# Kernel optimization log

Hardware: AMD Instinct MI355X
Metric: run time of the kernel (lower is better)

## Reference

```python
import jax, jax.numpy as jnp
import numpy as np

B = 64
IN_CH = 256
CH = 128
OUT_CH = 256
RES = 16
EMBED = 64
N_EMBED = 1024
N_PHYLO = 64          # n_phylo_channels; non-phylo = CH - N_PHYLO = 64
CODES = 16            # codes_per_phylolevel
LEVELS = 4            # n_phylolevels == n_levels_non_attribute
BETA = 0.25
FLAT_IN = N_PHYLO * RES * RES          # 16384
FLAT_Z = EMBED * CODES * LEVELS        # 4096


def setup_inputs() -> dict:
    key = jax.random.key(0)
    ks = jax.random.split(key, 16)
    s = 0.02
    return {
        "x": jax.random.normal(ks[0], (B, IN_CH, RES, RES), jnp.float32),
        "conv_in_w": jax.random.normal(ks[1], (IN_CH, CH), jnp.float32) * s,
        "conv_in_b": jnp.zeros((CH,), jnp.float32),
        "ln_p_g": jnp.ones((N_PHYLO, RES, RES), jnp.float32),
        "ln_p_b": jnp.zeros((N_PHYLO, RES, RES), jnp.float32),
        "W_in_p": jax.random.normal(ks[2], (FLAT_IN, FLAT_Z), jnp.float32) * s,
        "b_in_p": jnp.zeros((FLAT_Z,), jnp.float32),
        "ln_n_g": jnp.ones((CH - N_PHYLO, RES, RES), jnp.float32),
        "ln_n_b": jnp.zeros((CH - N_PHYLO, RES, RES), jnp.float32),
        "W_in_n": jax.random.normal(ks[3], (FLAT_IN, FLAT_Z), jnp.float32) * s,
        "b_in_n": jnp.zeros((FLAT_Z,), jnp.float32),
        "codebook": jax.random.uniform(ks[4], (N_EMBED, EMBED), jnp.float32, -1.0 / N_EMBED, 1.0 / N_EMBED),
        "W_out_p": jax.random.normal(ks[5], (FLAT_Z, FLAT_IN), jnp.float32) * s,
        "b_out_p": jnp.zeros((FLAT_IN,), jnp.float32),
        "W_out_n": jax.random.normal(ks[6], (FLAT_Z, FLAT_IN), jnp.float32) * s,
        "b_out_n": jnp.zeros((FLAT_IN,), jnp.float32),
        "conv_out_w": jax.random.normal(ks[7], (CH, OUT_CH), jnp.float32) * s,
        "conv_out_b": jnp.zeros((OUT_CH,), jnp.float32),
    }


def _layernorm(h, g, b, eps=1e-5):
    # normalize over (C,H,W) per sample, affine params shaped (C,H,W)
    m = jnp.mean(h, axis=(1, 2, 3), keepdims=True)
    v = jnp.var(h, axis=(1, 2, 3), keepdims=True)
    return (h - m) * jax.lax.rsqrt(v + eps) * g + b


def _quantize(z, codebook, beta=BETA):
    # z: (B, E, C, L) treated as (b, c, h, w) by taming VQ
    zp = jnp.transpose(z, (0, 2, 3, 1))                       # (B, C, L, E)
    zf = zp.reshape(-1, zp.shape[-1])                          # (B*C*L, E)
    d = (jnp.sum(zf * zf, axis=1, keepdims=True)
         - 2.0 * zf @ codebook.T
         + jnp.sum(codebook * codebook, axis=1)[None, :])      # (N_tok, n_embed)
    idx = jnp.argmin(d, axis=1)
    zq = codebook[idx].reshape(zp.shape)
    sg = jax.lax.stop_gradient
    loss = jnp.mean((sg(zq) - zp) ** 2) + beta * jnp.mean((zq - sg(zp)) ** 2)
    zq = zp + sg(zq - zp)                                      # straight-through
    return jnp.transpose(zq, (0, 3, 1, 2)), loss


def reference(x, conv_in_w, conv_in_b, ln_p_g, ln_p_b, W_in_p, b_in_p,
              ln_n_g, ln_n_b, W_in_n, b_in_n, codebook,
              W_out_p, b_out_p, W_out_n, b_out_n, conv_out_w, conv_out_b):
    # conv_in: 1x1 conv + SiLU
    h = jax.nn.silu(jnp.einsum('bchw,cd->bdhw', x, conv_in_w) + conv_in_b[None, :, None, None])
    h_phylo, h_img = h[:, :N_PHYLO], h[:, N_PHYLO:]

    # mlp_in (LayerNorm -> Flatten -> Linear -> Unflatten)
    z_p = (_layernorm(h_phylo, ln_p_g, ln_p_b).reshape(B, -1) @ W_in_p + b_in_p).reshape(B, EMBED, CODES, LEVELS)
    z_n = (_layernorm(h_img, ln_n_g, ln_n_b).reshape(B, -1) @ W_in_n + b_in_n).reshape(B, EMBED, CODES, LEVELS)

    zq_p, loss_p = _quantize(z_p, codebook)
    zq_n, loss_n = _quantize(z_n, codebook)
    quant_loss = loss_p + loss_n

    # mlp_out (Flatten -> Linear -> Unflatten)
    hout_p = (zq_p.reshape(B, -1) @ W_out_p + b_out_p).reshape(B, N_PHYLO, RES, RES)
    hout_n = (zq_n.reshape(B, -1) @ W_out_n + b_out_n).reshape(B, CH - N_PHYLO, RES, RES)
    h_ = jnp.concatenate([hout_p, hout_n], axis=1)

    # conv_out: SiLU -> 1x1 conv
    out = jnp.einsum('bchw,cd->bdhw', jax.nn.silu(h_), conv_out_w) + conv_out_b[None, :, None, None]
    return out, quant_loss
```

## Files before the change

kernel.cpp:

```cpp
#include <hip/hip_runtime.h>
#include <hip/hip_bf16.h>
#include <math.h>

#define BB 64
#define IN_CH 256
#define CH 128
#define OUT_CH 256
#define SP 256
#define EMBED 64
#define N_EMBED 1024
#define NPH 64
#define FLAT_IN 16384
#define FLAT_Z 4096

typedef short bf16x8 __attribute__((ext_vector_type(8)));
typedef float f32x4 __attribute__((ext_vector_type(4)));

__device__ __forceinline__ float silu_f(float x){ return x / (1.0f + expf(-x)); }

__device__ __forceinline__ void gl_lds16(const void* g, void* l){
  __builtin_amdgcn_global_load_lds(
      (const __attribute__((address_space(1))) void*)g,
      (__attribute__((address_space(3))) void*)l, 16, 0, 0);
}

__global__ __launch_bounds__(256) void k_fused_in(const float* __restrict__ x,
    const float* __restrict__ w1, const float* __restrict__ b1,
    const float* __restrict__ gp, const float* __restrict__ bp,
    const float* __restrict__ gn, const float* __restrict__ bnl,
    __hip_bfloat16* __restrict__ Ahi)
{
  int b = blockIdx.x, ws = blockIdx.y;
  int t = threadIdx.x;
  int d0 = ws*64;
  float acc[64];
  #pragma unroll
  for (int j=0;j<64;j++) acc[j] = b1[d0+j];
  const float* xb = x + (size_t)b*IN_CH*SP + t;
  for (int c=0;c<IN_CH;c++){
    float xv = xb[(size_t)c*SP];
    #pragma unroll
    for (int j=0;j<64;j++) acc[j] = fmaf(xv, w1[c*CH + d0 + j], acc[j]);
  }
  double s1=0.0, s2=0.0;
  #pragma unroll
  for (int j=0;j<64;j++){
    float v = silu_f(acc[j]);
    acc[j] = v;
    double dv = (double)v;
    s1 += dv; s2 += dv*dv;
  }
  __shared__ double l1[256], l2[256];
  l1[t]=s1; l2[t]=s2; __syncthreads();
  for (int s=128; s>0; s>>=1){
    if (t<s){ l1[t]+=l1[t+s]; l2[t]+=l2[t+s]; }
    __syncthreads();
  }
  double m = l1[0]/(double)FLAT_IN;
  double v = l2[0]/(double)FLAT_IN - m*m;
  float mf = (float)m;
  float rs = (float)(1.0/sqrt(v+1e-5));
  const float* g  = ws? gn : gp;
  const float* bb = ws? bnl: bp;
  __hip_bfloat16* oh = Ahi + ((size_t)ws*64 + b)*FLAT_IN;
  #pragma unroll 4
  for (int j=0;j<64;j++){
    int k = j*256 + t;
    float val = fmaf((acc[j]-mf)*rs, g[k], bb[k]);
    oh[k] = __float2bfloat16(val);
  }
}

template<int N, int K>
__global__ __launch_bounds__(256) void k_gemm_mfma(
    const __hip_bfloat16* __restrict__ A,
    const float* __restrict__ W0, const float* __restrict__ W1,
    float* __restrict__ part, int CHUNK, int KC)
{
  __shared__ float wlds[2*4096];
  __shared__ float alds[2*1024];
  int nt = blockIdx.x, kc = blockIdx.y, wsel = blockIdx.z;
  const float* W = wsel ? W1 : W0;
  int t = threadIdx.x;
  int wave = t >> 6, lane = t & 63;
  int rl = lane & 15;
  int g  = lane >> 4;
  int kg = g * 8;
  int nbase = nt*128;
  int k0 = kc*CHUNK;

  const __hip_bfloat16* Aw = A + (size_t)wsel*64*K;

  int s_lane = ((g&1)<<4) | ((g&2)<<1);
  int wbase0 = kg*128 + ((wave*32 + rl) ^ s_lane);
  int wbase1 = kg*128 + ((wave*32 + 16 + rl) ^ s_lane);
  int abyte[4];
  #pragma unroll
  for (int mf=0; mf<4; ++mf)
    abyte[mf] = (mf*16+rl)*64 + ((g ^ ((rl>>1)&3))<<4);

  int src_off[4]; int dst_base[4];
  #pragma unroll
  for (int i=0;i<4;i++){
    int fi = (i*4+wave)*256 + lane*4;
    int kl = fi>>7, nn = fi&127;
    int s = (((kl>>3)&1)<<4) | (((kl>>3)&2)<<1);
    src_off[i] = kl*N + nbase + (nn ^ s);
    dst_base[i] = (i*4+wave)*256;
  }
  size_t a_src = (size_t)(t>>2)*K + (size_t)(((t&3)^((t>>3)&3))*8);
  int a_dst = wave*256;

  f32x4 acc[4][2];
  #pragma unroll
  for (int mf=0; mf<4; ++mf){ acc[mf][0] = (f32x4){0,0,0,0}; acc[mf][1] = (f32x4){0,0,0,0}; }

  auto STAGE = [&](int buf, int ks){
    const float* Wr = W + (size_t)(k0 + ks*32)*N;
    float* lb = &wlds[buf*4096];
    #pragma unroll
    for (int i=0;i<4;i++) gl_lds16(Wr + src_off[i], lb + dst_base[i]);
    gl_lds16(Aw + a_src + (size_t)(k0 + ks*32), &alds[buf*1024] + a_dst);
  };

  int NT_ = CHUNK/32;
  STAGE(0, 0);

  for (int ks=0; ks<NT_; ++ks){
    int cur = ks & 1;
    int ksn = (ks+1 < NT_) ? ks+1 : ks;
    STAGE(cur^1, ksn);
    __builtin_amdgcn_sched_barrier(0);
    asm volatile("s_waitcnt vmcnt(5)" ::: "memory");
    __builtin_amdgcn_s_barrier();
    __builtin_amdgcn_sched_barrier(0);

    const float* lb = &wlds[cur*4096];
    const char* ab = (const char*)&alds[cur*1024];
    bf16x8 ah[4];
    #pragma unroll
    for (int mf=0; mf<4; ++mf) ah[mf] = *(const bf16x8*)(ab + abyte[mf]);
    float wv0[8], wv1[8];
    #pragma unroll
    for (int j=0;j<8;j++){ wv0[j] = lb[wbase0 + j*128]; wv1[j] = lb[wbase1 + j*128]; }
    bf16x8 bh0, bh1;
    #pragma unroll
    for (int j=0;j<8;j++){
      bh0[j] = __builtin_bit_cast(short, __float2bfloat16(wv0[j]));
      bh1[j] = __builtin_bit_cast(short, __float2bfloat16(wv1[j]));
    }
    #pragma unroll
    for (int mf=0; mf<4; ++mf){
      acc[mf][0] = __builtin_amdgcn_mfma_f32_16x16x32_bf16(ah[mf], bh0, acc[mf][0], 0,0,0);
      acc[mf][1] = __builtin_amdgcn_mfma_f32_16x16x32_bf16(ah[mf], bh1, acc[mf][1], 0,0,0);
    }
    __builtin_amdgcn_sched_barrier(0);
    __builtin_amdgcn_s_barrier();
  }
  asm volatile("s_waitcnt vmcnt(0)" ::: "memory");

  float* P = part + ((size_t)((wsel*KC + kc)*64))*N + nbase + wave*32 + rl;
  #pragma unroll
  for (int mf=0; mf<4; ++mf)
    #pragma unroll
    for (int f=0; f<2; ++f)
      #pragma unroll
      for (int r=0; r<4; ++r)
        P[((size_t)(mf*16 + g*4 + r))*N + f*16] = acc[mf][f][r];
}

__global__ __launch_bounds__(256) void k_zreduce(const float* __restrict__ part,
  const float* __restrict__ bp, const float* __restrict__ bn,
  float* __restrict__ z, int KC)
{
  int idx = blockIdx.x*256 + threadIdx.x;
  int ws = idx >> 18; int rem = idx & 262143;
  int m = rem >> 12; int n = rem & 4095;
  float s = (ws? bn: bp)[n];
  const float* p = part + ((size_t)ws*KC*64 + m)*4096 + n;
  for (int kc=0;kc<KC;kc++) s += p[(size_t)kc*64*4096];
  z[idx] = s;
}

__global__ __launch_bounds__(256) void k_cc(const float* __restrict__ cb, float* __restrict__ cc){
  int j = blockIdx.x*256 + threadIdx.x;
  if (j >= N_EMBED) return;
  float s=0.f;
  for (int e=0;e<EMBED;e++){ float c = cb[(size_t)j*EMBED+e]; s = fmaf(c,c,s); }
  cc[j]=s;
}

__global__ __launch_bounds__(256) void k_qscan(const float* __restrict__ z,
  const float* __restrict__ cb, const float* __restrict__ cc,
  float* __restrict__ bests, int* __restrict__ bestj)
{
  int r = blockIdx.x*256 + threadIdx.x;
  int cs = blockIdx.y;
  int ws = r>>12, rem = r&4095; int b = rem>>6, rr = rem&63;
  const float* zr = z + (size_t)ws*BB*FLAT_Z + (size_t)b*FLAT_Z + rr;
  float zr_[EMBED];
  #pragma unroll
  for (int e=0;e<EMBED;e++) zr_[e] = zr[(size_t)e*64];
  float best = 3.4e38f; int bj = 0;
  int j0 = cs*64;
  for (int jj=0;jj<64;jj++){
    int j = j0 + jj;
    const float* c = cb + (size_t)j*EMBED;
    float s1 = 0.f;
    #pragma unroll
    for (int e=0;e<EMBED;e++) s1 = fmaf(c[e], zr_[e], s1);
    float s = fmaf(-2.f, s1, cc[j]);
    if (s < best){ best = s; bj = j; }
  }
  bests[(size_t)cs*8192 + r] = best;
  bestj[(size_t)cs*8192 + r] = bj;
}

__global__ __launch_bounds__(256) void k_qfin(const float* __restrict__ z,
  const float* __restrict__ cb, const float* __restrict__ bests, const int* __restrict__ bestj,
  __hip_bfloat16* __restrict__ zqA, float* __restrict__ row_sse)
{
  int r = blockIdx.x*256 + threadIdx.x;
  float best = 3.4e38f; int bj = 0;
  for (int cs=0;cs<16;cs++){
    float v = bests[(size_t)cs*8192 + r];
    int j = bestj[(size_t)cs*8192 + r];
    if (v < best){ best=v; bj=j; }
  }
  int ws = r>>12, rem = r&4095; int b = rem>>6, rr = rem&63;
  const float* zr = z + (size_t)ws*BB*FLAT_Z + (size_t)b*FLAT_Z + rr;
  const float* c = cb + (size_t)bj*EMBED;
  __hip_bfloat16* zq = zqA + ((size_t)ws*64 + b)*FLAT_Z;
  float sse = 0.f;
  #pragma unroll
  for (int e=0;e<EMBED;e++){
    float cv = c[e];
    float zv = zr[(size_t)e*64];
    float d = cv - zv; sse = fmaf(d,d,sse);
    zq[(size_t)e*64 + rr] = __float2bfloat16(cv);
  }
  row_sse[r] = sse;
}

__global__ __launch_bounds__(256) void k_loss(const float* __restrict__ row_sse, float* __restrict__ out){
  __shared__ double l[256];
  double s=0.0;
  for (int i=threadIdx.x;i<8192;i+=256) s += (double)row_sse[i];
  l[threadIdx.x]=s; __syncthreads();
  for (int st=128;st>0;st>>=1){ if (threadIdx.x<st) l[threadIdx.x]+=l[threadIdx.x+st]; __syncthreads(); }
  if (threadIdx.x==0) out[(size_t)BB*OUT_CH*SP] = (float)(l[0]*1.25/262144.0);
}

__global__ __launch_bounds__(256) void k_hreduce(const float* __restrict__ part,
  const float* __restrict__ bp, const float* __restrict__ bn,
  float* __restrict__ hbuf, int KC)
{
  int idx = blockIdx.x*256 + threadIdx.x;
  int ws = idx >> 20; int rem = idx & 1048575;
  int m = rem >> 14; int n = rem & 16383;
  float s = (ws? bn: bp)[n];
  const float* p = part + ((size_t)ws*KC*64 + m)*16384 + n;
  for (int kc=0;kc<KC;kc++) s += p[(size_t)kc*64*16384];
  hbuf[((size_t)m*CH + ws*NPH + (n>>8))*SP + (n&255)] = s;
}

__global__ __launch_bounds__(256) void k_conv_out(const float* __restrict__ hbuf,
  const float* __restrict__ w2, const float* __restrict__ b2, float* __restrict__ out)
{
  int b = blockIdx.x, dg = blockIdx.y;
  int p = threadIdx.x;
  int d0 = dg*64;
  float acc[64];
  #pragma unroll
  for (int j=0;j<64;j++) acc[j]=b2[d0+j];
  const float* hb = hbuf + (size_t)b*CH*SP + p;
  for (int c=0;c<CH;c++){
    float hv = silu_f(hb[(size_t)c*SP]);
    #pragma unroll
    for (int j=0;j<64;j++) acc[j] = fmaf(hv, w2[c*OUT_CH + d0 + j], acc[j]);
  }
  float* ob = out + (size_t)b*OUT_CH*SP + (size_t)d0*SP + p;
  #pragma unroll
  for (int j=0;j<64;j++) ob[(size_t)j*SP] = acc[j];
}

extern "C" void kernel_launch(void* const* d_in, const int* in_sizes, int n_in,
                              void* d_out, int out_size, void* d_ws, size_t ws_size,
                              hipStream_t stream)
{
  const float* x   = (const float*)d_in[0];
  const float* w1  = (const float*)d_in[1];
  const float* b1  = (const float*)d_in[2];
  const float* gp  = (const float*)d_in[3];
  const float* bp  = (const float*)d_in[4];
  const float* Wip = (const float*)d_in[5];
  const float* bip = (const float*)d_in[6];
  const float* gn  = (const float*)d_in[7];
  const float* bnl = (const float*)d_in[8];
  const float* Win = (const float*)d_in[9];
  const float* bin = (const float*)d_in[10];
  const float* cb  = (const float*)d_in[11];
  const float* Wop = (const float*)d_in[12];
  const float* bop = (const float*)d_in[13];
  const float* Won = (const float*)d_in[14];
  const float* bon = (const float*)d_in[15];
  const float* w2  = (const float*)d_in[16];
  const float* b2  = (const float*)d_in[17];
  float* out = (float*)d_out;
  float* ws  = (float*)d_ws;

  __hip_bfloat16* Ahi = (__hip_bfloat16*)ws;
  float* z    = ws + 1048576;
  __hip_bfloat16* zqA = (__hip_bfloat16*)(ws + 1572864);
  float* hh   = ws + 1835008;
  float* cc   = ws + 3932160;
  float* sse  = ws + 3933184;
  float* bests= ws + 3941376;
  int*   bestj= (int*)(ws + 4072448);
  float* part = ws + 4203520;

  size_t wsf = ws_size/4;
  int KCe=16, KCd=4;
  if (wsf < (size_t)4203520 + 8388608) { KCe=8; KCd=2; }
  if (wsf < (size_t)4203520 + 4194304) { KCe=4; KCd=1; }

  k_fused_in<<<dim3(64,2),256,0,stream>>>(x,w1,b1,gp,bp,gn,bnl,Ahi);
  k_gemm_mfma<4096,16384><<<dim3(32,KCe,2),256,0,stream>>>(Ahi,Wip,Win,part,16384/KCe,KCe);
  k_zreduce<<<2048,256,0,stream>>>(part,bip,bin,z,KCe);
  k_cc<<<4,256,0,stream>>>(cb,cc);
  k_qscan<<<dim3(32,16),256,0,stream>>>(z,cb,cc,bests,bestj);
  k_qfin<<<32,256,0,stream>>>(z,cb,bests,bestj,zqA,sse);
  k_gemm_mfma<16384,4096><<<dim3(128,KCd,2),256,0,stream>>>(zqA,Wop,Won,part,4096/KCd,KCd);
  k_hreduce<<<8192,256,0,stream>>>(part,bop,bon,hh,KCd);
  k_conv_out<<<dim3(64,4),256,0,stream>>>(hh,w2,b2,out);
  k_loss<<<1,256,0,stream>>>(sse,out);
}
```

Measured before the change: 483.1 us.

## Give each wave a private LDS weight slice and load activations to registers

The GEMM mainloop now gives each wave its own LDS region holding only its 32 weight columns, so no block-wide s_barrier is needed per k-step. The A (bf16 activation) fragments are loaded straight from global memory into registers instead of being staged through LDS. The loop is unrolled by two with register double-buffering and a vmcnt wait in place of barriers. The goal is to remove barrier stalls and LDS traffic for A. In exchange, each wave redundantly fetches the same A rows from global memory, and the vmcnt counting has to be right for the new mix of loads.

Result: slower. 524.4 us (+8.5%).

```diff
diff --git a/kernel.cpp b/kernel.cpp
--- a/kernel.cpp
+++ b/kernel.cpp
@@ -77,72 +77,49 @@
     const float* __restrict__ W0, const float* __restrict__ W1,
     float* __restrict__ part, int CHUNK, int KC)
 {
-  __shared__ float wlds[2*4096];
-  __shared__ float alds[2*1024];
+  __shared__ float wlds[4*2048];
   int nt = blockIdx.x, kc = blockIdx.y, wsel = blockIdx.z;
   const float* W = wsel ? W1 : W0;
   int t = threadIdx.x;
   int wave = t >> 6, lane = t & 63;
   int rl = lane & 15;
   int g  = lane >> 4;
-  int kg = g * 8;
-  int nbase = nt*128;
+  int nbase = nt*128 + wave*32;
   int k0 = kc*CHUNK;
 
   const __hip_bfloat16* Aw = A + (size_t)wsel*64*K;
-
-  int s_lane = ((g&1)<<4) | ((g&2)<<1);
-  int wbase0 = kg*128 + ((wave*32 + rl) ^ s_lane);
-  int wbase1 = kg*128 + ((wave*32 + 16 + rl) ^ s_lane);
-  int abyte[4];
-  #pragma unroll
-  for (int mf=0; mf<4; ++mf)
-    abyte[mf] = (mf*16+rl)*64 + ((g ^ ((rl>>1)&3))<<4);
-
-  int src_off[4]; int dst_base[4];
-  #pragma unroll
-  for (int i=0;i<4;i++){
-    int fi = (i*4+wave)*256 + lane*4;
-    int kl = fi>>7, nn = fi&127;
-    int s = (((kl>>3)&1)<<4) | (((kl>>3)&2)<<1);
-    src_off[i] = kl*N + nbase + (nn ^ s);
-    dst_base[i] = (i*4+wave)*256;
-  }
-  size_t a_src = (size_t)(t>>2)*K + (size_t)(((t&3)^((t>>3)&3))*8);
-  int a_dst = wave*256;
+  float* wbuf = &wlds[wave*2048];
+
+  int src_off[4];
+  #pragma unroll
+  for (int i=0;i<4;i++)
+    src_off[i] = (i*8 + (lane>>3))*N + nbase + ((((lane&7)*4)) ^ ((i&1)<<4));
+
+  int rb0 = g*8*32 + ((rl)      ^ ((g&1)<<4));
+  int rb1 = g*8*32 + ((16 + rl) ^ ((g&1)<<4));
 
   f32x4 acc[4][2];
   #pragma unroll
   for (int mf=0; mf<4; ++mf){ acc[mf][0] = (f32x4){0,0,0,0}; acc[mf][1] = (f32x4){0,0,0,0}; }
 
-  auto STAGE = [&](int buf, int ks){
+  bf16x8 aA[4], aB[4];
+
+  auto STAGE = [&](int buf, int ks, bf16x8 (&areg)[4]){
     const float* Wr = W + (size_t)(k0 + ks*32)*N;
-    float* lb = &wlds[buf*4096];
-    #pragma unroll
-    for (int i=0;i<4;i++) gl_lds16(Wr + src_off[i], lb + dst_base[i]);
-    gl_lds16(Aw + a_src + (size_t)(k0 + ks*32), &alds[buf*1024] + a_dst);
+    float* dst = wbuf + buf*1024;
+    #pragma unroll
+    for (int i=0;i<4;i++) gl_lds16(Wr + src_off[i], dst + i*256);
+    size_t ko = (size_t)k0 + (size_t)ks*32 + g*8;
+    #pragma unroll
+    for (int mf=0; mf<4; ++mf)
+      areg[mf] = *(const bf16x8*)(Aw + (size_t)(mf*16+rl)*K + ko);
   };
 
-  int NT_ = CHUNK/32;
-  STAGE(0, 0);
-
-  for (int ks=0; ks<NT_; ++ks){
-    int cur = ks & 1;
-    int ksn = (ks+1 < NT_) ? ks+1 : ks;
-    STAGE(cur^1, ksn);
-    __builtin_amdgcn_sched_barrier(0);
-    asm volatile("s_waitcnt vmcnt(5)" ::: "memory");
-    __builtin_amdgcn_s_barrier();
-    __builtin_amdgcn_sched_barrier(0);
-
-    const float* lb = &wlds[cur*4096];
-    const char* ab = (const char*)&alds[cur*1024];
-    bf16x8 ah[4];
-    #pragma unroll
-    for (int mf=0; mf<4; ++mf) ah[mf] = *(const bf16x8*)(ab + abyte[mf]);
+  auto COMPUTE = [&](int buf, bf16x8 (&areg)[4]){
+    const float* lb = wbuf + buf*1024;
     float wv0[8], wv1[8];
     #pragma unroll
-    for (int j=0;j<8;j++){ wv0[j] = lb[wbase0 + j*128]; wv1[j] = lb[wbase1 + j*128]; }
+    for (int j=0;j<8;j++){ wv0[j] = lb[rb0 + j*32]; wv1[j] = lb[rb1 + j*32]; }
     bf16x8 bh0, bh1;
     #pragma unroll
     for (int j=0;j<8;j++){
@@ -151,15 +128,29 @@
     }
     #pragma unroll
     for (int mf=0; mf<4; ++mf){
-      acc[mf][0] = __builtin_amdgcn_mfma_f32_16x16x32_bf16(ah[mf], bh0, acc[mf][0], 0,0,0);
-      acc[mf][1] = __builtin_amdgcn_mfma_f32_16x16x32_bf16(ah[mf], bh1, acc[mf][1], 0,0,0);
+      acc[mf][0] = __builtin_amdgcn_mfma_f32_16x16x32_bf16(areg[mf], bh0, acc[mf][0], 0,0,0);
+      acc[mf][1] = __builtin_amdgcn_mfma_f32_16x16x32_bf16(areg[mf], bh1, acc[mf][1], 0,0,0);
     }
+  };
+
+  int NT_ = CHUNK/32;
+  STAGE(0, 0, aA);
+  for (int ks2=0; ks2<NT_/2; ++ks2){
+    STAGE(1, 2*ks2+1, aB);
     __builtin_amdgcn_sched_barrier(0);
-    __builtin_amdgcn_s_barrier();
+    asm volatile("s_waitcnt vmcnt(8)" ::: "memory");
+    __builtin_amdgcn_sched_barrier(0);
+    COMPUTE(0, aA);
+    int ksn = (2*ks2+2 < NT_) ? 2*ks2+2 : 2*ks2+1;
+    STAGE(0, ksn, aA);
+    __builtin_amdgcn_sched_barrier(0);
+    asm volatile("s_waitcnt vmcnt(8)" ::: "memory");
+    __builtin_amdgcn_sched_barrier(0);
+    COMPUTE(1, aB);
   }
   asm volatile("s_waitcnt vmcnt(0)" ::: "memory");
 
-  float* P = part + ((size_t)((wsel*KC + kc)*64))*N + nbase + wave*32 + rl;
+  float* P = part + ((size_t)((wsel*KC + kc)*64))*N + nbase + rl;
   #pragma unroll
   for (int mf=0; mf<4; ++mf)
     #pragma unroll
```
